# Optimization experiments

Hardware: AMD Instinct MI355X
Metric: run time of the kernel (lower is better)

## Reference

```python
import jax, jax.numpy as jnp
import numpy as np

NUM_HEADS = 12
FEATURE_DIM = 16
HEAD_DIM = 128
EPS = 1e-12


def taylor_map(x):
    # x: [b, h, t, d] -> [b, h, t, 1 + d + d*d] (2nd-order Taylor features of exp)
    d = x.shape[-1]
    r2 = jnp.asarray(np.sqrt(2.0), x.dtype)
    rd = jnp.asarray(np.sqrt(d), x.dtype)
    rrd = jnp.asarray(np.sqrt(np.sqrt(d)), x.dtype)
    x2 = (x[..., :, None] * x[..., None, :]).reshape(x.shape[:-1] + (d * d,)) / r2
    ones = jnp.ones(x.shape[:-1] + (1,), x.dtype)
    return jnp.concatenate([ones, x / rrd, x2 / rd], axis=-1)


def setup_inputs() -> dict:
    key = jax.random.key(0)
    ks = jax.random.split(key, 5)
    b, t, hid = 2, 2048, 1536
    scale = 0.02
    return {
        "hidden_states": jax.random.normal(ks[0], (b, t, hid), jnp.float32),
        "Wq": jax.random.normal(ks[1], (NUM_HEADS * FEATURE_DIM, hid), jnp.float32) * scale,
        "Wk": jax.random.normal(ks[2], (NUM_HEADS * FEATURE_DIM, hid), jnp.float32) * scale,
        "Wv": jax.random.normal(ks[3], (NUM_HEADS * HEAD_DIM, hid), jnp.float32) * scale,
        "Wo": jax.random.normal(ks[4], (hid, NUM_HEADS * HEAD_DIM), jnp.float32) * scale,
    }


def reference(hidden_states, Wq, Wk, Wv, Wo):
    b, t, _ = hidden_states.shape
    H, dk, dv = NUM_HEADS, FEATURE_DIM, HEAD_DIM
    # projections (torch Linear: x @ W^T), split heads -> [b, h, t, d]
    q = (hidden_states @ Wq.T).reshape(b, t, H, dk).transpose(0, 2, 1, 3)
    k = (hidden_states @ Wk.T).reshape(b, t, H, dk).transpose(0, 2, 1, 3)
    v = (hidden_states @ Wv.T).reshape(b, t, H, dv).transpose(0, 2, 1, 3)
    qf = taylor_map(q)  # [b, h, t, D], D = 1 + dk + dk^2
    kf = taylor_map(k)
    # causal kernelized attention: identical math to cumsum-of-outer-products form
    S = jnp.einsum("bhtd,bhsd->bhts", qf, kf)  # [b, h, t, t]
    mask = jnp.tril(jnp.ones((t, t), bool))
    S = jnp.where(mask, S, jnp.zeros((), S.dtype))
    num = jnp.einsum("bhts,bhse->bhte", S, v)  # [b, h, t, dv]
    den = S.sum(-1) + EPS  # [b, h, t]
    y = num / den[..., None]
    y = y.transpose(0, 2, 1, 3).reshape(b, t, H * dv)
    return y @ Wo.T
```

## Files before the change

### kernel.cpp

```cpp
#include <hip/hip_runtime.h>

#define B 2
#define T 2048
#define HID 1536
#define NH 12
#define DK 16
#define DV 128
#define BT (B * T)
#define EPS 1e-12f

typedef __attribute__((ext_vector_type(8))) short bf16x8;
typedef __attribute__((ext_vector_type(4))) float f32x4;

__device__ __forceinline__ unsigned short f2bf(float f) {
    unsigned int u = __float_as_uint(f);
    u += 0x7FFFu + ((u >> 16) & 1u);
    return (unsigned short)(u >> 16);
}

__global__ __launch_bounds__(256) void cvt_all(const float* __restrict__ hs,
                                               const float* __restrict__ Wq,
                                               const float* __restrict__ Wk,
                                               const float* __restrict__ Wv,
                                               const float* __restrict__ Wo,
                                               unsigned short* __restrict__ hsb,
                                               unsigned short* __restrict__ wqk,
                                               unsigned short* __restrict__ wvb,
                                               unsigned short* __restrict__ wob) {
    int bx = blockIdx.x;
    const float* src;
    unsigned short* dst;
    if (bx < 3072)      { src = hs; dst = hsb; }
    else if (bx < 3216) { src = Wq; dst = wqk;          bx -= 3072; }
    else if (bx < 3360) { src = Wk; dst = wqk + 294912; bx -= 3216; }
    else if (bx < 4512) { src = Wv; dst = wvb;          bx -= 3360; }
    else                { src = Wo; dst = wob;          bx -= 4512; }
    const int i = (bx * 256 + threadIdx.x) * 8;
    float4 a = *(const float4*)(src + i);
    float4 b = *(const float4*)(src + i + 4);
    *(ushort4*)(dst + i)     = make_ushort4(f2bf(a.x), f2bf(a.y), f2bf(a.z), f2bf(a.w));
    *(ushort4*)(dst + i + 4) = make_ushort4(f2bf(b.x), f2bf(b.y), f2bf(b.z), f2bf(b.w));
}

__device__ __forceinline__ void gemm_tile_bf16(const unsigned short* __restrict__ A,
                                               const unsigned short* __restrict__ Bm,
                                               unsigned short* __restrict__ C,
                                               int m0, int n0, int K, int ldc,
                                               unsigned short* As, unsigned short* Bs) {
    const int tid = threadIdx.x;
    const int wave = tid >> 6, lane = tid & 63;
    const int wm = (wave & 1) * 64, wn = (wave >> 1) * 64;
    const int fr = lane & 15;
    const int fk = (lane >> 4) * 8;

    f32x4 acc[4][4];
#pragma unroll
    for (int i = 0; i < 4; ++i)
#pragma unroll
        for (int j = 0; j < 4; ++j) acc[i][j] = (f32x4)0.f;

    const int c0 = tid, c1 = tid + 256;
    const int r0 = c0 >> 2, q0 = (c0 & 3) * 8;
    const int r1 = c1 >> 2, q1 = (c1 & 3) * 8;

    for (int k0 = 0; k0 < K; k0 += 32) {
        __builtin_amdgcn_global_load_lds(
            (const __attribute__((address_space(1))) void*)(A + (size_t)(m0 + r0) * K + k0 + q0),
            (__attribute__((address_space(3))) void*)(As + c0 * 8), 16, 0, 0);
        __builtin_amdgcn_global_load_lds(
            (const __attribute__((address_space(1))) void*)(A + (size_t)(m0 + r1) * K + k0 + q1),
            (__attribute__((address_space(3))) void*)(As + c1 * 8), 16, 0, 0);
        __builtin_amdgcn_global_load_lds(
            (const __attribute__((address_space(1))) void*)(Bm + (size_t)(n0 + r0) * K + k0 + q0),
            (__attribute__((address_space(3))) void*)(Bs + c0 * 8), 16, 0, 0);
        __builtin_amdgcn_global_load_lds(
            (const __attribute__((address_space(1))) void*)(Bm + (size_t)(n0 + r1) * K + k0 + q1),
            (__attribute__((address_space(3))) void*)(Bs + c1 * 8), 16, 0, 0);
        __syncthreads();

        bf16x8 af[4], bfr[4];
#pragma unroll
        for (int mb = 0; mb < 4; ++mb)
            af[mb] = *(const bf16x8*)(As + (wm + mb * 16 + fr) * 32 + fk);
#pragma unroll
        for (int nb = 0; nb < 4; ++nb)
            bfr[nb] = *(const bf16x8*)(Bs + (wn + nb * 16 + fr) * 32 + fk);
#pragma unroll
        for (int mb = 0; mb < 4; ++mb)
#pragma unroll
            for (int nb = 0; nb < 4; ++nb)
                acc[mb][nb] = __builtin_amdgcn_mfma_f32_16x16x32_bf16(
                    af[mb], bfr[nb], acc[mb][nb], 0, 0, 0);
        __syncthreads();
    }

    const int orow = (lane >> 4) * 4;
#pragma unroll
    for (int nb = 0; nb < 4; ++nb) {
        const int col = n0 + wn + nb * 16 + fr;
#pragma unroll
        for (int mb = 0; mb < 4; ++mb) {
            const int row = m0 + wm + mb * 16 + orow;
#pragma unroll
            for (int r = 0; r < 4; ++r)
                C[(size_t)(row + r) * ldc + col] = f2bf(acc[mb][nb][r]);
        }
    }
}

__global__ __launch_bounds__(256) void proj_qkv(const unsigned short* __restrict__ hsb,
                                                const unsigned short* __restrict__ wqk,
                                                const unsigned short* __restrict__ wvb,
                                                unsigned short* __restrict__ qkb,
                                                unsigned short* __restrict__ vtg) {
    __shared__ unsigned short As[128 * 32];
    __shared__ unsigned short Bs[128 * 32];
    const int bx = blockIdx.x;
    if (bx < 96) {
        gemm_tile_bf16(hsb, wqk, qkb, (bx / 3) * 128, (bx % 3) * 128, HID, 384, As, Bs);
    } else {
        const int vid = bx - 96;
        const int grp = vid / 48, sub = vid % 48;
        const int n_t = grp * 4 + (sub & 3), m_t = sub >> 2;
        gemm_tile_bf16(wvb, hsb, vtg, m_t * 128, n_t * 128, HID, BT, As, Bs);
    }
}

__global__ __launch_bounds__(256) void proj_out(const unsigned short* __restrict__ A,
                                                const unsigned short* __restrict__ Bm,
                                                float* __restrict__ C) {
    __shared__ unsigned short As[128 * 32];
    __shared__ unsigned short Bs[128 * 32];
    const int tid = threadIdx.x;
    const int m0 = blockIdx.y * 128;
    const int n0 = blockIdx.x * 128;
    const int wave = tid >> 6, lane = tid & 63;
    const int wm = (wave & 1) * 64, wn = (wave >> 1) * 64;
    const int fr = lane & 15;
    const int fk = (lane >> 4) * 8;
    const int K = HID;

    f32x4 acc[4][4];
#pragma unroll
    for (int i = 0; i < 4; ++i)
#pragma unroll
        for (int j = 0; j < 4; ++j) acc[i][j] = (f32x4)0.f;

    const int c0 = tid, c1 = tid + 256;
    const int r0 = c0 >> 2, q0 = (c0 & 3) * 8;
    const int r1 = c1 >> 2, q1 = (c1 & 3) * 8;

    for (int k0 = 0; k0 < K; k0 += 32) {
        __builtin_amdgcn_global_load_lds(
            (const __attribute__((address_space(1))) void*)(A + (size_t)(m0 + r0) * K + k0 + q0),
            (__attribute__((address_space(3))) void*)(As + c0 * 8), 16, 0, 0);
        __builtin_amdgcn_global_load_lds(
            (const __attribute__((address_space(1))) void*)(A + (size_t)(m0 + r1) * K + k0 + q1),
            (__attribute__((address_space(3))) void*)(As + c1 * 8), 16, 0, 0);
        __builtin_amdgcn_global_load_lds(
            (const __attribute__((address_space(1))) void*)(Bm + (size_t)(n0 + r0) * K + k0 + q0),
            (__attribute__((address_space(3))) void*)(Bs + c0 * 8), 16, 0, 0);
        __builtin_amdgcn_global_load_lds(
            (const __attribute__((address_space(1))) void*)(Bm + (size_t)(n0 + r1) * K + k0 + q1),
            (__attribute__((address_space(3))) void*)(Bs + c1 * 8), 16, 0, 0);
        __syncthreads();

        bf16x8 af[4], bfr[4];
#pragma unroll
        for (int mb = 0; mb < 4; ++mb)
            af[mb] = *(const bf16x8*)(As + (wm + mb * 16 + fr) * 32 + fk);
#pragma unroll
        for (int nb = 0; nb < 4; ++nb)
            bfr[nb] = *(const bf16x8*)(Bs + (wn + nb * 16 + fr) * 32 + fk);
#pragma unroll
        for (int mb = 0; mb < 4; ++mb)
#pragma unroll
            for (int nb = 0; nb < 4; ++nb)
                acc[mb][nb] = __builtin_amdgcn_mfma_f32_16x16x32_bf16(
                    af[mb], bfr[nb], acc[mb][nb], 0, 0, 0);
        __syncthreads();
    }

    const int orow = (lane >> 4) * 4;
#pragma unroll
    for (int nb = 0; nb < 4; ++nb) {
        const int col = n0 + wn + nb * 16 + fr;
#pragma unroll
        for (int mb = 0; mb < 4; ++mb) {
            const int row = m0 + wm + mb * 16 + orow;
#pragma unroll
            for (int r = 0; r < 4; ++r)
                C[(size_t)(row + r) * HID + col] = acc[mb][nb][r];
        }
    }
}

__global__ __launch_bounds__(256) void based_attn_mfma(const unsigned short* __restrict__ qk,
                                                       const unsigned short* __restrict__ vt,
                                                       unsigned short* __restrict__ yb) {
    const int bx = blockIdx.x;
    const int qt = (T / 64 - 1) - (bx / (NH * B));
    const int hb = bx % (NH * B);
    const int h  = hb >> 1;
    const int bi = hb & 1;
    const int tid = threadIdx.x;
    const int wave = tid >> 6, lane = tid & 63;
    const int fr = lane & 15, quad = lane >> 4;
    const int fk = quad * 8;
    const int fkk = (quad & 1) * 8;

    __shared__ __attribute__((aligned(16))) unsigned short ss[2][64][72];
    __shared__ float den_lds[64];
    if (tid < 64) den_lds[tid] = 0.f;

    const bf16x8 zf = {};
    bf16x8 qf[4];
#pragma unroll
    for (int nt = 0; nt < 4; ++nt) {
        qf[nt] = zf;
        if (quad < 2)
            qf[nt] = *(const bf16x8*)&qk[(size_t)(bi * T + qt * 64 + nt * 16 + fr) * 384
                                         + h * DK + fk];
    }

    f32x4 oacc[2][4];
#pragma unroll
    for (int mt = 0; mt < 2; ++mt)
#pragma unroll
        for (int nt = 0; nt < 4; ++nt) oacc[mt][nt] = (f32x4)0.f;
    float denp[4] = {0.f, 0.f, 0.f, 0.f};

    const unsigned short* kbase = qk + (size_t)(bi * T + wave * 16 + fr) * 384 + 192 + h * DK + fkk;
    const unsigned short* vbase0 = vt + (size_t)(h * DV + wave * 32 + fr) * BT + bi * T + fk;
    const unsigned short* vbase1 = vbase0 + (size_t)16 * BT;

    bf16x8 kf_n = *(const bf16x8*)kbase;
    bf16x8 vf_n[2][2];
    vf_n[0][0] = *(const bf16x8*)(vbase0);
    vf_n[0][1] = *(const bf16x8*)(vbase0 + 32);
    vf_n[1][0] = *(const bf16x8*)(vbase1);
    vf_n[1][1] = *(const bf16x8*)(vbase1 + 32);

    for (int kt = 0; kt <= qt; ++kt) {
        const int bsel = kt & 1;
        const bf16x8 kf = kf_n;
        bf16x8 vf[2][2];
        vf[0][0] = vf_n[0][0]; vf[0][1] = vf_n[0][1];
        vf[1][0] = vf_n[1][0]; vf[1][1] = vf_n[1][1];

        {
            const int ktn = (kt < qt) ? kt + 1 : qt;
            kf_n = *(const bf16x8*)(kbase + (size_t)ktn * 64 * 384);
            const int off = ktn * 64;
            vf_n[0][0] = *(const bf16x8*)(vbase0 + off);
            vf_n[0][1] = *(const bf16x8*)(vbase0 + off + 32);
            vf_n[1][0] = *(const bf16x8*)(vbase1 + off);
            vf_n[1][1] = *(const bf16x8*)(vbase1 + off + 32);
        }

        f32x4 sa[4];
#pragma unroll
        for (int nt = 0; nt < 4; ++nt)
            sa[nt] = __builtin_amdgcn_mfma_f32_16x16x32_bf16(kf, qf[nt], (f32x4)0.f, 0, 0, 0);

#pragma unroll
        for (int nt = 0; nt < 4; ++nt) {
            const int i = nt * 16 + fr;
            float sv[4];
#pragma unroll
            for (int r = 0; r < 4; ++r) {
                const float a = sa[nt][r];
                sv[r] = fmaf(a, fmaf(a, 1.f / 32.f, 0.25f), 1.f);
            }
            if (kt == qt) {
#pragma unroll
                for (int r = 0; r < 4; ++r) {
                    const int j = wave * 16 + quad * 4 + r;
                    if (j > i) sv[r] = 0.f;
                }
            }
            denp[nt] += sv[0] + sv[1] + sv[2] + sv[3];
            uint2 pk;
            pk.x = (__float_as_uint(sv[0]) >> 16) | (__float_as_uint(sv[1]) & 0xFFFF0000u);
            pk.y = (__float_as_uint(sv[2]) >> 16) | (__float_as_uint(sv[3]) & 0xFFFF0000u);
            *(uint2*)&ss[bsel][i][wave * 16 + quad * 4] = pk;
        }
        __syncthreads();

#pragma unroll
        for (int k2 = 0; k2 < 2; ++k2) {
            bf16x8 sf[4];
#pragma unroll
            for (int nt = 0; nt < 4; ++nt)
                sf[nt] = *(const bf16x8*)&ss[bsel][nt * 16 + fr][k2 * 32 + fk];
#pragma unroll
            for (int mt = 0; mt < 2; ++mt)
#pragma unroll
                for (int nt = 0; nt < 4; ++nt)
                    oacc[mt][nt] = __builtin_amdgcn_mfma_f32_16x16x32_bf16(
                        vf[mt][k2], sf[nt], oacc[mt][nt], 0, 0, 0);
        }
    }

#pragma unroll
    for (int nt = 0; nt < 4; ++nt) {
        float v = denp[nt];
        v += __shfl_xor(v, 16);
        v += __shfl_xor(v, 32);
        if (quad == 0) atomicAdd(&den_lds[nt * 16 + fr], v);
    }
    __syncthreads();

#pragma unroll
    for (int nt = 0; nt < 4; ++nt) {
        const int i = nt * 16 + fr;
        const float rd = 1.f / (den_lds[i] + EPS);
        const size_t rowbase = (size_t)(bi * T + qt * 64 + i) * (NH * DV) + h * DV;
#pragma unroll
        for (int mt = 0; mt < 2; ++mt) {
            const int c = wave * 32 + mt * 16 + quad * 4;
            const f32x4 o = oacc[mt][nt];
            *(ushort4*)&yb[rowbase + c] = make_ushort4(f2bf(o[0] * rd), f2bf(o[1] * rd),
                                                       f2bf(o[2] * rd), f2bf(o[3] * rd));
        }
    }
}

extern "C" void kernel_launch(void* const* d_in, const int* in_sizes, int n_in,
                              void* d_out, int out_size, void* d_ws, size_t ws_size,
                              hipStream_t stream) {
    (void)in_sizes; (void)n_in; (void)out_size; (void)ws_size;
    const float* hs = (const float*)d_in[0];
    const float* Wq = (const float*)d_in[1];
    const float* Wk = (const float*)d_in[2];
    const float* Wv = (const float*)d_in[3];
    const float* Wo = (const float*)d_in[4];
    float* out = (float*)d_out;

    unsigned short* hsb = (unsigned short*)d_ws;
    unsigned short* wqk = hsb + (size_t)BT * HID;
    unsigned short* wvb = wqk + (size_t)384 * HID;
    unsigned short* wob = wvb + (size_t)HID * HID;
    unsigned short* qkb = wob + (size_t)HID * HID;
    unsigned short* vtg = qkb + (size_t)BT * 384;
    unsigned short* ybb = vtg + (size_t)HID * BT;

    dim3 blk(256);
    cvt_all<<<dim3(5664), blk, 0, stream>>>(hs, Wq, Wk, Wv, Wo, hsb, wqk, wvb, wob);

    proj_qkv<<<dim3(480), blk, 0, stream>>>(hsb, wqk, wvb, qkb, vtg);

    based_attn_mfma<<<dim3(T / 64 * NH * B), blk, 0, stream>>>(qkb, vtg, ybb);

    proj_out<<<dim3(12, 32), blk, 0, stream>>>(ybb, wob, out);
}
```

Baseline: 213.5 us.

## Split attention key tiles across waves, remove per-tile LDS score exchange

The attention kernel now uses 16x16x16 bf16 MFMAs so each wave's score fragment can feed the PV MFMA directly from registers as the B operand. Each wave owns a 16-key slice and all 128 value columns, so the per-iteration LDS round-trip and __syncthreads are gone. Partial outputs from the four waves are then combined with LDS float atomics at the end. In exchange it issues twice as many MFMA instructions with half the K depth, quadruples the accumulator registers (32 f32x4), and adds a zeroed 128x66 float LDS buffer plus an atomic reduction. It also uses hardware bf16 packing and a launch-bounds occupancy hint.

```diff
diff --git a/kernel.cpp b/kernel.cpp
--- a/kernel.cpp
+++ b/kernel.cpp
@@ -10,12 +10,30 @@
 #define EPS 1e-12f
 
 typedef __attribute__((ext_vector_type(8))) short bf16x8;
+typedef __attribute__((ext_vector_type(4))) short bf16x4;
 typedef __attribute__((ext_vector_type(4))) float f32x4;
 
 __device__ __forceinline__ unsigned short f2bf(float f) {
     unsigned int u = __float_as_uint(f);
     u += 0x7FFFu + ((u >> 16) & 1u);
     return (unsigned short)(u >> 16);
+}
+
+#if __has_builtin(__builtin_amdgcn_mfma_f32_16x16x16bf16_1k)
+__device__ __forceinline__ f32x4 mfma16(bf16x4 a, bf16x4 b, f32x4 c) {
+    return __builtin_amdgcn_mfma_f32_16x16x16bf16_1k(a, b, c, 0, 0, 0);
+}
+#else
+__device__ __forceinline__ f32x4 mfma16(bf16x4 a, bf16x4 b, f32x4 c) {
+    asm("v_mfma_f32_16x16x16_bf16 %0, %1, %2, %0" : "+v"(c) : "v"(a), "v"(b));
+    return c;
+}
+#endif
+
+__device__ __forceinline__ unsigned int cvt_pk_bf16(float lo, float hi) {
+    unsigned int r;
+    asm("v_cvt_pk_bf16_f32 %0, %1, %2" : "=v"(r) : "v"(lo), "v"(hi));
+    return r;
 }
 
 __global__ __launch_bounds__(256) void cvt_all(const float* __restrict__ hs,
@@ -195,9 +213,9 @@
     }
 }
 
-__global__ __launch_bounds__(256) void based_attn_mfma(const unsigned short* __restrict__ qk,
-                                                       const unsigned short* __restrict__ vt,
-                                                       unsigned short* __restrict__ yb) {
+__global__ __launch_bounds__(256, 2) void based_attn_mfma(const unsigned short* __restrict__ qk,
+                                                          const unsigned short* __restrict__ vt,
+                                                          unsigned short* __restrict__ yb) {
     const int bx = blockIdx.x;
     const int qt = (T / 64 - 1) - (bx / (NH * B));
     const int hb = bx % (NH * B);
@@ -206,100 +224,80 @@
     const int tid = threadIdx.x;
     const int wave = tid >> 6, lane = tid & 63;
     const int fr = lane & 15, quad = lane >> 4;
-    const int fk = quad * 8;
-    const int fkk = (quad & 1) * 8;
-
-    __shared__ __attribute__((aligned(16))) unsigned short ss[2][64][72];
+
+    __shared__ float olds[128][66];
     __shared__ float den_lds[64];
+
+    for (int idx = tid; idx < 128 * 66; idx += 256) (&olds[0][0])[idx] = 0.f;
     if (tid < 64) den_lds[tid] = 0.f;
-
-    const bf16x8 zf = {};
-    bf16x8 qf[4];
-#pragma unroll
-    for (int nt = 0; nt < 4; ++nt) {
-        qf[nt] = zf;
-        if (quad < 2)
-            qf[nt] = *(const bf16x8*)&qk[(size_t)(bi * T + qt * 64 + nt * 16 + fr) * 384
-                                         + h * DK + fk];
-    }
-
-    f32x4 oacc[2][4];
-#pragma unroll
-    for (int mt = 0; mt < 2; ++mt)
+    __syncthreads();
+
+    bf16x4 qf[4];
+#pragma unroll
+    for (int nt = 0; nt < 4; ++nt)
+        qf[nt] = *(const bf16x4*)(qk + (size_t)(bi * T + qt * 64 + nt * 16 + fr) * 384
+                                  + h * DK + quad * 4);
+
+    f32x4 oacc[8][4];
+#pragma unroll
+    for (int mt = 0; mt < 8; ++mt)
 #pragma unroll
         for (int nt = 0; nt < 4; ++nt) oacc[mt][nt] = (f32x4)0.f;
     float denp[4] = {0.f, 0.f, 0.f, 0.f};
 
-    const unsigned short* kbase = qk + (size_t)(bi * T + wave * 16 + fr) * 384 + 192 + h * DK + fkk;
-    const unsigned short* vbase0 = vt + (size_t)(h * DV + wave * 32 + fr) * BT + bi * T + fk;
-    const unsigned short* vbase1 = vbase0 + (size_t)16 * BT;
-
-    bf16x8 kf_n = *(const bf16x8*)kbase;
-    bf16x8 vf_n[2][2];
-    vf_n[0][0] = *(const bf16x8*)(vbase0);
-    vf_n[0][1] = *(const bf16x8*)(vbase0 + 32);
-    vf_n[1][0] = *(const bf16x8*)(vbase1);
-    vf_n[1][1] = *(const bf16x8*)(vbase1 + 32);
+    const unsigned short* kbase = qk + (size_t)(bi * T + wave * 16 + fr) * 384
+                                  + 192 + h * DK + quad * 4;
+    const unsigned short* vbase = vt + (size_t)(h * DV + fr) * BT
+                                  + bi * T + wave * 16 + quad * 4;
+
+    bf16x4 kf_n = *(const bf16x4*)kbase;
+    bf16x4 vf_n[8];
+#pragma unroll
+    for (int mt = 0; mt < 8; ++mt)
+        vf_n[mt] = *(const bf16x4*)(vbase + (size_t)mt * 16 * BT);
 
     for (int kt = 0; kt <= qt; ++kt) {
-        const int bsel = kt & 1;
-        const bf16x8 kf = kf_n;
-        bf16x8 vf[2][2];
-        vf[0][0] = vf_n[0][0]; vf[0][1] = vf_n[0][1];
-        vf[1][0] = vf_n[1][0]; vf[1][1] = vf_n[1][1];
+        const bf16x4 kf = kf_n;
+        bf16x4 vf[8];
+#pragma unroll
+        for (int mt = 0; mt < 8; ++mt) vf[mt] = vf_n[mt];
 
         {
             const int ktn = (kt < qt) ? kt + 1 : qt;
-            kf_n = *(const bf16x8*)(kbase + (size_t)ktn * 64 * 384);
-            const int off = ktn * 64;
-            vf_n[0][0] = *(const bf16x8*)(vbase0 + off);
-            vf_n[0][1] = *(const bf16x8*)(vbase0 + off + 32);
-            vf_n[1][0] = *(const bf16x8*)(vbase1 + off);
-            vf_n[1][1] = *(const bf16x8*)(vbase1 + off + 32);
-        }
-
-        f32x4 sa[4];
-#pragma unroll
-        for (int nt = 0; nt < 4; ++nt)
-            sa[nt] = __builtin_amdgcn_mfma_f32_16x16x32_bf16(kf, qf[nt], (f32x4)0.f, 0, 0, 0);
-
+            kf_n = *(const bf16x4*)(kbase + (size_t)ktn * 64 * 384);
+#pragma unroll
+            for (int mt = 0; mt < 8; ++mt)
+                vf_n[mt] = *(const bf16x4*)(vbase + (size_t)mt * 16 * BT + ktn * 64);
+        }
+
+        bf16x4 sb[4];
 #pragma unroll
         for (int nt = 0; nt < 4; ++nt) {
-            const int i = nt * 16 + fr;
+            f32x4 sa = mfma16(kf, qf[nt], (f32x4)0.f);
             float sv[4];
 #pragma unroll
             for (int r = 0; r < 4; ++r) {
-                const float a = sa[nt][r];
+                const float a = sa[r];
                 sv[r] = fmaf(a, fmaf(a, 1.f / 32.f, 0.25f), 1.f);
             }
             if (kt == qt) {
-#pragma unroll
-                for (int r = 0; r < 4; ++r) {
-                    const int j = wave * 16 + quad * 4 + r;
-                    if (j > i) sv[r] = 0.f;
-                }
+                const int i = nt * 16 + fr;
+#pragma unroll
+                for (int r = 0; r < 4; ++r)
+                    if (wave * 16 + quad * 4 + r > i) sv[r] = 0.f;
             }
-            denp[nt] += sv[0] + sv[1] + sv[2] + sv[3];
-            uint2 pk;
-            pk.x = (__float_as_uint(sv[0]) >> 16) | (__float_as_uint(sv[1]) & 0xFFFF0000u);
-            pk.y = (__float_as_uint(sv[2]) >> 16) | (__float_as_uint(sv[3]) & 0xFFFF0000u);
-            *(uint2*)&ss[bsel][i][wave * 16 + quad * 4] = pk;
-        }
-        __syncthreads();
-
-#pragma unroll
-        for (int k2 = 0; k2 < 2; ++k2) {
-            bf16x8 sf[4];
+            denp[nt] += (sv[0] + sv[1]) + (sv[2] + sv[3]);
+            union { uint2 u; bf16x4 v; } pk;
+            pk.u.x = cvt_pk_bf16(sv[0], sv[1]);
+            pk.u.y = cvt_pk_bf16(sv[2], sv[3]);
+            sb[nt] = pk.v;
+        }
+
+#pragma unroll
+        for (int mt = 0; mt < 8; ++mt)
 #pragma unroll
             for (int nt = 0; nt < 4; ++nt)
-                sf[nt] = *(const bf16x8*)&ss[bsel][nt * 16 + fr][k2 * 32 + fk];
-#pragma unroll
-            for (int mt = 0; mt < 2; ++mt)
-#pragma unroll
-                for (int nt = 0; nt < 4; ++nt)
-                    oacc[mt][nt] = __builtin_amdgcn_mfma_f32_16x16x32_bf16(
-                        vf[mt][k2], sf[nt], oacc[mt][nt], 0, 0, 0);
-        }
+                oacc[mt][nt] = mfma16(vf[mt], sb[nt], oacc[mt][nt]);
     }
 
 #pragma unroll
@@ -309,19 +307,29 @@
         v += __shfl_xor(v, 32);
         if (quad == 0) atomicAdd(&den_lds[nt * 16 + fr], v);
     }
+
+#pragma unroll
+    for (int mt = 0; mt < 8; ++mt)
+#pragma unroll
+        for (int nt = 0; nt < 4; ++nt)
+#pragma unroll
+            for (int r = 0; r < 4; ++r)
+                atomicAdd(&olds[mt * 16 + quad * 4 + r][nt * 16 + fr], oacc[mt][nt][r]);
     __syncthreads();
 
-#pragma unroll
-    for (int nt = 0; nt < 4; ++nt) {
-        const int i = nt * 16 + fr;
+    {
+        const int i = tid & 63;
+        const int cb = (tid >> 6) * 32;
         const float rd = 1.f / (den_lds[i] + EPS);
         const size_t rowbase = (size_t)(bi * T + qt * 64 + i) * (NH * DV) + h * DV;
 #pragma unroll
-        for (int mt = 0; mt < 2; ++mt) {
-            const int c = wave * 32 + mt * 16 + quad * 4;
-            const f32x4 o = oacc[mt][nt];
-            *(ushort4*)&yb[rowbase + c] = make_ushort4(f2bf(o[0] * rd), f2bf(o[1] * rd),
-                                                       f2bf(o[2] * rd), f2bf(o[3] * rd));
+        for (int cc = 0; cc < 32; cc += 4) {
+            ushort4 o;
+            o.x = f2bf(olds[cb + cc + 0][i] * rd);
+            o.y = f2bf(olds[cb + cc + 1][i] * rd);
+            o.z = f2bf(olds[cb + cc + 2][i] * rd);
+            o.w = f2bf(olds[cb + cc + 3][i] * rd);
+            *(ushort4*)&yb[rowbase + cb + cc] = o;
         }
     }
 }
```

Result: slower. 381.6 us (+78.7%).

## Split attention value dimension across two blocks to double grid parallelism

Applied to the files above, without the earlier changes.

Each attention block now computes only half of the 128-wide value dimension, so the grid holds twice as many blocks (1536 instead of 768). The goal is better occupancy and load balance across the CUs for the causal, triangular workload. In exchange, the QK score computation, the Taylor feature map and the denominator are done twice, once per half, which adds redundant MFMA and LDS work.

```diff
diff --git a/kernel.cpp b/kernel.cpp
--- a/kernel.cpp
+++ b/kernel.cpp
@@ -199,10 +199,11 @@
                                                        const unsigned short* __restrict__ vt,
                                                        unsigned short* __restrict__ yb) {
     const int bx = blockIdx.x;
-    const int qt = (T / 64 - 1) - (bx / (NH * B));
-    const int hb = bx % (NH * B);
-    const int h  = hb >> 1;
-    const int bi = hb & 1;
+    const int qt = (T / 64 - 1) - (bx / (NH * B * 2));
+    const int rem = bx % (NH * B * 2);
+    const int h   = rem >> 2;
+    const int dvh = (rem >> 1) & 1;
+    const int bi  = rem & 1;
     const int tid = threadIdx.x;
     const int wave = tid >> 6, lane = tid & 63;
     const int fr = lane & 15, quad = lane >> 4;
@@ -223,39 +224,32 @@
                                          + h * DK + fk];
     }
 
-    f32x4 oacc[2][4];
-#pragma unroll
-    for (int mt = 0; mt < 2; ++mt)
-#pragma unroll
-        for (int nt = 0; nt < 4; ++nt) oacc[mt][nt] = (f32x4)0.f;
+    f32x4 oacc[4];
+#pragma unroll
+    for (int nt = 0; nt < 4; ++nt) oacc[nt] = (f32x4)0.f;
     float denp[4] = {0.f, 0.f, 0.f, 0.f};
 
     const unsigned short* kbase = qk + (size_t)(bi * T + wave * 16 + fr) * 384 + 192 + h * DK + fkk;
-    const unsigned short* vbase0 = vt + (size_t)(h * DV + wave * 32 + fr) * BT + bi * T + fk;
-    const unsigned short* vbase1 = vbase0 + (size_t)16 * BT;
+    const unsigned short* vbase = vt + (size_t)(h * DV + dvh * 64 + wave * 16 + fr) * BT
+                                  + bi * T + fk;
 
     bf16x8 kf_n = *(const bf16x8*)kbase;
-    bf16x8 vf_n[2][2];
-    vf_n[0][0] = *(const bf16x8*)(vbase0);
-    vf_n[0][1] = *(const bf16x8*)(vbase0 + 32);
-    vf_n[1][0] = *(const bf16x8*)(vbase1);
-    vf_n[1][1] = *(const bf16x8*)(vbase1 + 32);
+    bf16x8 vf_n[2];
+    vf_n[0] = *(const bf16x8*)(vbase);
+    vf_n[1] = *(const bf16x8*)(vbase + 32);
 
     for (int kt = 0; kt <= qt; ++kt) {
         const int bsel = kt & 1;
         const bf16x8 kf = kf_n;
-        bf16x8 vf[2][2];
-        vf[0][0] = vf_n[0][0]; vf[0][1] = vf_n[0][1];
-        vf[1][0] = vf_n[1][0]; vf[1][1] = vf_n[1][1];
+        bf16x8 vf[2];
+        vf[0] = vf_n[0]; vf[1] = vf_n[1];
 
         {
             const int ktn = (kt < qt) ? kt + 1 : qt;
             kf_n = *(const bf16x8*)(kbase + (size_t)ktn * 64 * 384);
             const int off = ktn * 64;
-            vf_n[0][0] = *(const bf16x8*)(vbase0 + off);
-            vf_n[0][1] = *(const bf16x8*)(vbase0 + off + 32);
-            vf_n[1][0] = *(const bf16x8*)(vbase1 + off);
-            vf_n[1][1] = *(const bf16x8*)(vbase1 + off + 32);
+            vf_n[0] = *(const bf16x8*)(vbase + off);
+            vf_n[1] = *(const bf16x8*)(vbase + off + 32);
         }
 
         f32x4 sa[4];
@@ -294,11 +288,9 @@
             for (int nt = 0; nt < 4; ++nt)
                 sf[nt] = *(const bf16x8*)&ss[bsel][nt * 16 + fr][k2 * 32 + fk];
 #pragma unroll
-            for (int mt = 0; mt < 2; ++mt)
-#pragma unroll
-                for (int nt = 0; nt < 4; ++nt)
-                    oacc[mt][nt] = __builtin_amdgcn_mfma_f32_16x16x32_bf16(
-                        vf[mt][k2], sf[nt], oacc[mt][nt], 0, 0, 0);
+            for (int nt = 0; nt < 4; ++nt)
+                oacc[nt] = __builtin_amdgcn_mfma_f32_16x16x32_bf16(
+                    vf[k2], sf[nt], oacc[nt], 0, 0, 0);
         }
     }
 
@@ -315,14 +307,11 @@
     for (int nt = 0; nt < 4; ++nt) {
         const int i = nt * 16 + fr;
         const float rd = 1.f / (den_lds[i] + EPS);
-        const size_t rowbase = (size_t)(bi * T + qt * 64 + i) * (NH * DV) + h * DV;
-#pragma unroll
-        for (int mt = 0; mt < 2; ++mt) {
-            const int c = wave * 32 + mt * 16 + quad * 4;
-            const f32x4 o = oacc[mt][nt];
-            *(ushort4*)&yb[rowbase + c] = make_ushort4(f2bf(o[0] * rd), f2bf(o[1] * rd),
-                                                       f2bf(o[2] * rd), f2bf(o[3] * rd));
-        }
+        const size_t rowbase = (size_t)(bi * T + qt * 64 + i) * (NH * DV) + h * DV + dvh * 64;
+        const int c = wave * 16 + quad * 4;
+        const f32x4 o = oacc[nt];
+        *(ushort4*)&yb[rowbase + c] = make_ushort4(f2bf(o[0] * rd), f2bf(o[1] * rd),
+                                                   f2bf(o[2] * rd), f2bf(o[3] * rd));
     }
 }
 
@@ -350,7 +339,7 @@
 
     proj_qkv<<<dim3(480), blk, 0, stream>>>(hsb, wqk, wvb, qkb, vtg);
 
-    based_attn_mfma<<<dim3(T / 64 * NH * B), blk, 0, stream>>>(qkb, vtg, ybb);
+    based_attn_mfma<<<dim3(T / 64 * NH * B * 2), blk, 0, stream>>>(qkb, vtg, ybb);
 
     proj_out<<<dim3(12, 32), blk, 0, stream>>>(ybb, wob, out);
 }
```

Result: no change. 215.3 us (+0.8%).

## Halve attention query tile to 32 rows and use hardware bf16 pack

Applied to the files above, without the earlier changes.

The attention kernel now gives each block a 32-row query tile instead of 64, which doubles the grid to 1536 blocks so more CUs have work and the causal triangle is balanced more finely. Key/value tiles stay 64 wide, so the causal mask offset is now computed relative to the 32-row tile. The manual truncating bf16 pack of scores is replaced by the v_cvt_pk_bf16_f32 instruction, which rounds instead of truncating. The cost is that K/V reloads and the total MFMA work on the last, partly masked tile grow relative to the useful work.

```diff
diff --git a/kernel.cpp b/kernel.cpp
--- a/kernel.cpp
+++ b/kernel.cpp
@@ -16,6 +16,12 @@
     unsigned int u = __float_as_uint(f);
     u += 0x7FFFu + ((u >> 16) & 1u);
     return (unsigned short)(u >> 16);
+}
+
+__device__ __forceinline__ unsigned int cvt_pk_bf16(float lo, float hi) {
+    unsigned int r;
+    asm("v_cvt_pk_bf16_f32 %0, %1, %2" : "=v"(r) : "v"(lo), "v"(hi));
+    return r;
 }
 
 __global__ __launch_bounds__(256) void cvt_all(const float* __restrict__ hs,
@@ -199,7 +205,7 @@
                                                        const unsigned short* __restrict__ vt,
                                                        unsigned short* __restrict__ yb) {
     const int bx = blockIdx.x;
-    const int qt = (T / 64 - 1) - (bx / (NH * B));
+    const int t  = (T / 32 - 1) - (bx / (NH * B));
     const int hb = bx % (NH * B);
     const int h  = hb >> 1;
     const int bi = hb & 1;
@@ -208,27 +214,28 @@
     const int fr = lane & 15, quad = lane >> 4;
     const int fk = quad * 8;
     const int fkk = (quad & 1) * 8;
-
-    __shared__ __attribute__((aligned(16))) unsigned short ss[2][64][72];
-    __shared__ float den_lds[64];
-    if (tid < 64) den_lds[tid] = 0.f;
+    const int kt_max = t >> 1;
+
+    __shared__ __attribute__((aligned(16))) unsigned short ss[2][32][72];
+    __shared__ float den_lds[32];
+    if (tid < 32) den_lds[tid] = 0.f;
 
     const bf16x8 zf = {};
-    bf16x8 qf[4];
-#pragma unroll
-    for (int nt = 0; nt < 4; ++nt) {
+    bf16x8 qf[2];
+#pragma unroll
+    for (int nt = 0; nt < 2; ++nt) {
         qf[nt] = zf;
         if (quad < 2)
-            qf[nt] = *(const bf16x8*)&qk[(size_t)(bi * T + qt * 64 + nt * 16 + fr) * 384
+            qf[nt] = *(const bf16x8*)&qk[(size_t)(bi * T + t * 32 + nt * 16 + fr) * 384
                                          + h * DK + fk];
     }
 
-    f32x4 oacc[2][4];
+    f32x4 oacc[2][2];
 #pragma unroll
     for (int mt = 0; mt < 2; ++mt)
 #pragma unroll
-        for (int nt = 0; nt < 4; ++nt) oacc[mt][nt] = (f32x4)0.f;
-    float denp[4] = {0.f, 0.f, 0.f, 0.f};
+        for (int nt = 0; nt < 2; ++nt) oacc[mt][nt] = (f32x4)0.f;
+    float denp[2] = {0.f, 0.f};
 
     const unsigned short* kbase = qk + (size_t)(bi * T + wave * 16 + fr) * 384 + 192 + h * DK + fkk;
     const unsigned short* vbase0 = vt + (size_t)(h * DV + wave * 32 + fr) * BT + bi * T + fk;
@@ -241,7 +248,7 @@
     vf_n[1][0] = *(const bf16x8*)(vbase1);
     vf_n[1][1] = *(const bf16x8*)(vbase1 + 32);
 
-    for (int kt = 0; kt <= qt; ++kt) {
+    for (int kt = 0; kt <= kt_max; ++kt) {
         const int bsel = kt & 1;
         const bf16x8 kf = kf_n;
         bf16x8 vf[2][2];
@@ -249,7 +256,7 @@
         vf[1][0] = vf_n[1][0]; vf[1][1] = vf_n[1][1];
 
         {
-            const int ktn = (kt < qt) ? kt + 1 : qt;
+            const int ktn = (kt < kt_max) ? kt + 1 : kt_max;
             kf_n = *(const bf16x8*)(kbase + (size_t)ktn * 64 * 384);
             const int off = ktn * 64;
             vf_n[0][0] = *(const bf16x8*)(vbase0 + off);
@@ -258,13 +265,14 @@
             vf_n[1][1] = *(const bf16x8*)(vbase1 + off + 32);
         }
 
-        f32x4 sa[4];
-#pragma unroll
-        for (int nt = 0; nt < 4; ++nt)
+        f32x4 sa[2];
+#pragma unroll
+        for (int nt = 0; nt < 2; ++nt)
             sa[nt] = __builtin_amdgcn_mfma_f32_16x16x32_bf16(kf, qf[nt], (f32x4)0.f, 0, 0, 0);
 
-#pragma unroll
-        for (int nt = 0; nt < 4; ++nt) {
+        const int jbase = kt * 64 + wave * 16 + quad * 4 - t * 32;
+#pragma unroll
+        for (int nt = 0; nt < 2; ++nt) {
             const int i = nt * 16 + fr;
             float sv[4];
 #pragma unroll
@@ -272,38 +280,36 @@
                 const float a = sa[nt][r];
                 sv[r] = fmaf(a, fmaf(a, 1.f / 32.f, 0.25f), 1.f);
             }
-            if (kt == qt) {
-#pragma unroll
-                for (int r = 0; r < 4; ++r) {
-                    const int j = wave * 16 + quad * 4 + r;
-                    if (j > i) sv[r] = 0.f;
-                }
+            if (kt == kt_max) {
+#pragma unroll
+                for (int r = 0; r < 4; ++r)
+                    if (jbase + r > i) sv[r] = 0.f;
             }
-            denp[nt] += sv[0] + sv[1] + sv[2] + sv[3];
+            denp[nt] += (sv[0] + sv[1]) + (sv[2] + sv[3]);
             uint2 pk;
-            pk.x = (__float_as_uint(sv[0]) >> 16) | (__float_as_uint(sv[1]) & 0xFFFF0000u);
-            pk.y = (__float_as_uint(sv[2]) >> 16) | (__float_as_uint(sv[3]) & 0xFFFF0000u);
+            pk.x = cvt_pk_bf16(sv[0], sv[1]);
+            pk.y = cvt_pk_bf16(sv[2], sv[3]);
             *(uint2*)&ss[bsel][i][wave * 16 + quad * 4] = pk;
         }
         __syncthreads();
 
 #pragma unroll
         for (int k2 = 0; k2 < 2; ++k2) {
-            bf16x8 sf[4];
-#pragma unroll
-            for (int nt = 0; nt < 4; ++nt)
+            bf16x8 sf[2];
+#pragma unroll
+            for (int nt = 0; nt < 2; ++nt)
                 sf[nt] = *(const bf16x8*)&ss[bsel][nt * 16 + fr][k2 * 32 + fk];
 #pragma unroll
             for (int mt = 0; mt < 2; ++mt)
 #pragma unroll
-                for (int nt = 0; nt < 4; ++nt)
+                for (int nt = 0; nt < 2; ++nt)
                     oacc[mt][nt] = __builtin_amdgcn_mfma_f32_16x16x32_bf16(
                         vf[mt][k2], sf[nt], oacc[mt][nt], 0, 0, 0);
         }
     }
 
 #pragma unroll
-    for (int nt = 0; nt < 4; ++nt) {
+    for (int nt = 0; nt < 2; ++nt) {
         float v = denp[nt];
         v += __shfl_xor(v, 16);
         v += __shfl_xor(v, 32);
@@ -312,10 +318,10 @@
     __syncthreads();
 
 #pragma unroll
-    for (int nt = 0; nt < 4; ++nt) {
+    for (int nt = 0; nt < 2; ++nt) {
         const int i = nt * 16 + fr;
         const float rd = 1.f / (den_lds[i] + EPS);
-        const size_t rowbase = (size_t)(bi * T + qt * 64 + i) * (NH * DV) + h * DV;
+        const size_t rowbase = (size_t)(bi * T + t * 32 + i) * (NH * DV) + h * DV;
 #pragma unroll
         for (int mt = 0; mt < 2; ++mt) {
             const int c = wave * 32 + mt * 16 + quad * 4;
@@ -350,7 +356,7 @@
 
     proj_qkv<<<dim3(480), blk, 0, stream>>>(hsb, wqk, wvb, qkb, vtg);
 
-    based_attn_mfma<<<dim3(T / 64 * NH * B), blk, 0, stream>>>(qkb, vtg, ybb);
+    based_attn_mfma<<<dim3(T / 32 * NH * B), blk, 0, stream>>>(qkb, vtg, ybb);
 
     proj_out<<<dim3(12, 32), blk, 0, stream>>>(ybb, wob, out);
 }
```

Result: slower. 232.2 us (+8.8%).
